# Performance work log

Measured on AMD Instinct MI355X. Metric: run time of the kernel, lower is better.

The kernel has to match this reference:

```python
import jax, jax.numpy as jnp
import numpy as np

B, T, I, H, O = 128, 512, 256, 512, 256


def setup_inputs() -> dict:
    key = jax.random.key(0)
    ks = jax.random.split(key, 12)
    s = 1.0 / np.sqrt(H)  # torch nn.GRUCell/Linear-style uniform init scale
    u = lambda k, shape: jax.random.uniform(k, shape, jnp.float32, -s, s)
    return {
        "x": jax.random.normal(ks[0], (B, T, I), jnp.float32),
        "h0": jax.random.normal(ks[1], (B, H), jnp.float32),
        "W_ih0": u(ks[2], (3 * H, I)),
        "W_hh0": u(ks[3], (3 * H, H)),
        "b_ih0": u(ks[4], (3 * H,)),
        "b_hh0": u(ks[5], (3 * H,)),
        "W_ih1": u(ks[6], (3 * H, H)),
        "W_hh1": u(ks[7], (3 * H, H)),
        "b_ih1": u(ks[8], (3 * H,)),
        "b_hh1": u(ks[9], (3 * H,)),
        "W_out": u(ks[10], (O, H)),
        "b_out": u(ks[11], (O,)),
    }


def _cell(inp, h, W_ih, W_hh, b_ih, b_hh):
    # Standard GRU cell (PyTorch gate order: r, z, n)
    gi = inp @ W_ih.T + b_ih  # [B, 3H]
    gh = h @ W_hh.T + b_hh    # [B, 3H]
    i_r, i_z, i_n = jnp.split(gi, 3, axis=-1)
    h_r, h_z, h_n = jnp.split(gh, 3, axis=-1)
    r = jax.nn.sigmoid(i_r + h_r)
    z = jax.nn.sigmoid(i_z + h_z)
    n = jnp.tanh(i_n + r * h_n)
    return (1.0 - z) * n + z * h


def reference(x, h0, W_ih0, W_hh0, b_ih0, b_hh0, W_ih1, W_hh1, b_ih1, b_hh1, W_out, b_out):
    def step(h, x_t):
        h = _cell(x_t, h, W_ih0, W_hh0, b_ih0, b_hh0)
        # Source quirk: a SINGLE hidden state is shared across stacked layers,
        # so layer 1 receives h both as input and as previous hidden state.
        h = _cell(h, h, W_ih1, W_hh1, b_ih1, b_hh1)
        y = h @ W_out.T + b_out  # [B, O]
        return h, y

    _, Y = jax.lax.scan(step, h0, jnp.swapaxes(x, 0, 1))  # Y: [T, B, O]
    return jnp.swapaxes(Y, 0, 1)  # [B, T, O]
```

## Files before the change

### kernel.cpp

```cpp
#include <hip/hip_runtime.h>


typedef short s16x8 __attribute__((ext_vector_type(8)));
typedef float f32x4 __attribute__((ext_vector_type(4)));
typedef unsigned short u16;
typedef unsigned int u32;

#define MFMA(a, b, c) __builtin_amdgcn_mfma_f32_16x16x32_bf16((a), (b), (c), 0, 0, 0)

static constexpr int NBLK = 128;
static constexpr int LDS_WROWS = 112;
static constexpr int LDS_STRIDE = 520;
static constexpr int LDS_BYTES = LDS_WROWS * LDS_STRIDE * 2 + 2 * 512 * 4;
static constexpr int OFF_FA = 0, OFF_FB = 8192, OFF_GA = 16384, OFF_GB = 17408;
static constexpr int FLAGS_U32 = 18432;

__device__ __forceinline__ u16 f2bf(float f) {
  unsigned u = __builtin_bit_cast(unsigned, f);
  u = u + 0x7fffu + ((u >> 16) & 1u);
  return (u16)(u >> 16);
}
__device__ __forceinline__ float sigm(float x) { return 1.f / (1.f + __expf(-x)); }
__device__ __forceinline__ float tanh_f(float x) { return 1.f - 2.f / (1.f + __expf(2.f * x)); }

__device__ __forceinline__ s16x8 scload16(const u16* p) {
  s16x8 v;
  asm volatile("global_load_dwordx4 %0, %1, off sc0 sc1" : "=v"(v) : "v"(p));
  return v;
}
__device__ __forceinline__ void scstore_u16(u16* p, u16 v) {
  unsigned vv = v;
  asm volatile("global_store_short %0, %1, off sc0 sc1" :: "v"(p), "v"(vv) : "memory");
}
__device__ __forceinline__ u32 scload_u32(const u32* p) {
  u32 v;
  asm volatile("global_load_dword %0, %1, off sc0 sc1\n\ts_waitcnt vmcnt(0)"
               : "=v"(v) : "v"(p) : "memory");
  return v;
}
__device__ __forceinline__ void scstore_u32(u32* p, u32 v) {
  asm volatile("global_store_dword %0, %1, off sc0 sc1" :: "v"(p), "v"(v) : "memory");
}
#define VWAIT0()                                        \
  do {                                                  \
    asm volatile("s_waitcnt vmcnt(0)" ::: "memory");    \
    __builtin_amdgcn_sched_barrier(0);                  \
  } while (0)
#define DRAIN_ALL()                                              \
  do {                                                           \
    asm volatile("s_waitcnt vmcnt(0) lgkmcnt(0)" ::: "memory");  \
    __builtin_amdgcn_sched_barrier(0);                           \
  } while (0)

__device__ __forceinline__ void gather64(const u32* base, u32 val, int l) {
  for (;;) {
    u32 v = scload_u32(base + l * 32);
    if (__all(v >= val)) break;
    __builtin_amdgcn_s_sleep(2);
  }
}
__device__ __forceinline__ void pollgo(const u32* p, u32 val) {
  for (;;) {
    u32 v = scload_u32(p);
    if (v >= val) break;
    __builtin_amdgcn_s_sleep(4);
  }
}

__global__ void prep_kernel(const float* __restrict__ W_ih0, const float* __restrict__ W_hh0,
                            const float* __restrict__ W_ih1, const float* __restrict__ W_hh1,
                            const float* __restrict__ W_out, const float* __restrict__ h0,
                            u16* __restrict__ WL0, u16* __restrict__ WL1,
                            u16* __restrict__ WOB, u16* __restrict__ ring1,
                            u32* __restrict__ flags) {
  const int n0 = 1536 * 768, n1 = 2048 * 512, n2 = 256 * 512, n3 = 128 * 512;
  const int total = n0 + n1 + n2 + n3 + FLAGS_U32;
  for (int i = blockIdx.x * blockDim.x + threadIdx.x; i < total; i += gridDim.x * blockDim.x) {
    if (i < n0) {
      int row = i / 768, c = i % 768;
      float v = (c < 256) ? W_ih0[row * 256 + c] : W_hh0[row * 512 + (c - 256)];
      WL0[i] = f2bf(v);
    } else if (i < n0 + n1) {
      int k2 = i - n0;
      int row = k2 / 512, k = k2 % 512;
      int strip = row >> 9, j = row & 511;
      float v;
      if (strip == 0)      v = W_ih1[j * 512 + k] + W_hh1[j * 512 + k];
      else if (strip == 1) v = W_ih1[(512 + j) * 512 + k] + W_hh1[(512 + j) * 512 + k];
      else if (strip == 2) v = W_ih1[(1024 + j) * 512 + k];
      else                 v = W_hh1[(1024 + j) * 512 + k];
      WL1[k2] = f2bf(v);
    } else if (i < n0 + n1 + n2) {
      int k2 = i - n0 - n1;
      WOB[k2] = f2bf(W_out[k2]);
    } else if (i < n0 + n1 + n2 + n3) {
      int k2 = i - n0 - n1 - n2;
      ring1[k2] = f2bf(h0[k2]);
    } else {
      flags[i - n0 - n1 - n2 - n3] = 0u;
    }
  }
}

__global__ __launch_bounds__(256) void gru_persist(
    const float* __restrict__ x, const float* __restrict__ h0,
    const float* __restrict__ b_ih0, const float* __restrict__ b_hh0,
    const float* __restrict__ b_ih1, const float* __restrict__ b_hh1,
    const float* __restrict__ b_out,
    const u16* __restrict__ WL0, const u16* __restrict__ WL1, const u16* __restrict__ WOB,
    u16* __restrict__ ring,
    u16* __restrict__ hlb,
    float* __restrict__ Y, u32* __restrict__ flags) {
  extern __shared__ u16 smem[];
  float* h_f32  = (float*)(smem + LDS_WROWS * LDS_STRIDE);
  float* hl_f32 = h_f32 + 512;

  const int blk = blockIdx.x;
  const int m = blk >> 5;
  const int s = blk & 31;
  const int w = threadIdx.x >> 6, l = threadIdx.x & 63;
  const int l15 = l & 15, l4 = l >> 4;

  for (int idx = threadIdx.x; idx < LDS_WROWS * 512; idx += 256) {
    int row = idx >> 9, k = idx & 511;
    u16 v;
    if (row < 48) {
      int g = row >> 4, jj = row & 15;
      v = WL0[(size_t)(g * 512 + s * 16 + jj) * 768 + 256 + k];
    } else {
      int rr = row - 48, g = rr >> 4, jj = rr & 15;
      v = WL1[(size_t)(g * 512 + s * 16 + jj) * 512 + k];
    }
    smem[row * LDS_STRIDE + k] = v;
  }
  for (int idx = threadIdx.x; idx < 512; idx += 256) {
    int rr = idx >> 4, cc = idx & 15;
    h_f32[idx] = h0[(size_t)(32 * m + rr) * 512 + s * 16 + cc];
  }
  __syncthreads();

  const int jg = s * 16 + l15;
  const float br0 = b_ih0[jg] + b_hh0[jg];
  const float bz0 = b_ih0[512 + jg] + b_hh0[512 + jg];
  const float bni0 = b_ih0[1024 + jg], bnh0 = b_hh0[1024 + jg];
  const float br1 = b_ih1[jg] + b_hh1[jg];
  const float bz1 = b_ih1[512 + jg] + b_hh1[512 + jg];
  const float bni1 = b_ih1[1024 + jg], bnh1 = b_hh1[1024 + jg];

  const u16* wxr = WL0 + (size_t)jg * 768 + l4 * 8;
  const u16* wxz = WL0 + (size_t)(512 + jg) * 768 + l4 * 8;
  const u16* wxn = WL0 + (size_t)(1024 + jg) * 768 + l4 * 8;
  const u16* lr  = smem + (0 * 16 + l15) * LDS_STRIDE + l4 * 8;
  const u16* lz  = smem + (1 * 16 + l15) * LDS_STRIDE + l4 * 8;
  const u16* ln  = smem + (2 * 16 + l15) * LDS_STRIDE + l4 * 8;
  const u16* m10 = smem + (48 + 0 * 16 + l15) * LDS_STRIDE + l4 * 8;
  const u16* m11 = smem + (48 + 1 * 16 + l15) * LDS_STRIDE + l4 * 8;
  const u16* m12 = smem + (48 + 2 * 16 + l15) * LDS_STRIDE + l4 * 8;
  const u16* m13 = smem + (48 + 3 * 16 + l15) * LDS_STRIDE + l4 * 8;

  u32* fA = flags + OFF_FA + m * 2048;
  u32* fB = flags + OFF_FB + m * 2048;
  u32* gA = flags + OFF_GA + m * 256;
  u32* gB = flags + OFF_GB + m * 256;

  if (w < 2) {
    const int amt = w;
    const int arow = 32 * m + amt * 16 + l15;
    u32* myfA = fA + (s * 2 + amt) * 32;
    const u32* mygo = gB + (s & 7) * 32;
    const int yo = (s & 15) * 16 + l15;
    const float ybo = b_out[yo];
    const u16* ywv = WOB + (size_t)yo * 512 + l4 * 8;

    for (int t = 0; t < 512; ++t) {
      const u16* ringc = ring + (size_t)((t + 1) & 1) * 65536;

      if (t > 0) {
        if (s == 0) {
          gather64(fB, (u32)t, l);
          if (w == 0 && l < 8) scstore_u32(gB + l * 32, (u32)t);
        } else {
          pollgo(mygo, (u32)t);
        }
        __builtin_amdgcn_sched_barrier(0);
      }

      s16x8 hb[16];
      const u16* hr = ringc + (size_t)arow * 512 + l4 * 8;
      #pragma unroll
      for (int kt = 0; kt < 16; ++kt) hb[kt] = scload16(hr + kt * 32);

      f32x4 aR = {0,0,0,0}, aZ = {0,0,0,0}, aNI = {0,0,0,0}, aNH = {0,0,0,0};
      const float* xr = x + ((size_t)arow * 512 + t) * 256 + l4 * 8;
      #pragma unroll
      for (int kt = 0; kt < 8; ++kt) {
        float4 u = *(const float4*)(xr + kt * 32);
        float4 v = *(const float4*)(xr + kt * 32 + 4);
        s16x8 a;
        a[0]=f2bf(u.x); a[1]=f2bf(u.y); a[2]=f2bf(u.z); a[3]=f2bf(u.w);
        a[4]=f2bf(v.x); a[5]=f2bf(v.y); a[6]=f2bf(v.z); a[7]=f2bf(v.w);
        aR  = MFMA(a, *(const s16x8*)(wxr + kt * 32), aR);
        aZ  = MFMA(a, *(const s16x8*)(wxz + kt * 32), aZ);
        aNI = MFMA(a, *(const s16x8*)(wxn + kt * 32), aNI);
      }
      VWAIT0();
      #pragma unroll
      for (int kt = 0; kt < 16; ++kt) {
        aR  = MFMA(hb[kt], *(const s16x8*)(lr + kt * 32), aR);
        aZ  = MFMA(hb[kt], *(const s16x8*)(lz + kt * 32), aZ);
        aNH = MFMA(hb[kt], *(const s16x8*)(ln + kt * 32), aNH);
      }

      #pragma unroll
      for (int j = 0; j < 4; ++j) {
        int rr = amt * 16 + l4 * 4 + j;
        float r = sigm(aR[j] + br0), z = sigm(aZ[j] + bz0);
        float n = tanh_f(aNI[j] + bni0 + r * (aNH[j] + bnh0));
        float h = (1.f - z) * n + z * h_f32[rr * 16 + l15];
        hl_f32[rr * 16 + l15] = h;
        scstore_u16(hlb + (size_t)(32 * m + rr) * 512 + jg, f2bf(h));
      }
      DRAIN_ALL();
      if (l == 0) scstore_u32(myfA, (u32)(t + 1));

      if (s < 16 && t > 0) {
        f32x4 acc = {0,0,0,0};
        #pragma unroll
        for (int kt = 0; kt < 16; ++kt)
          acc = MFMA(hb[kt], *(const s16x8*)(ywv + kt * 32), acc);
        #pragma unroll
        for (int j = 0; j < 4; ++j)
          Y[((size_t)(32 * m + amt * 16 + l4 * 4 + j) * 512 + (t - 1)) * 256 + yo]
              = acc[j] + ybo;
      }
    }

    if (s == 0) {
      gather64(fB, 512u, l);
      if (w == 0 && l < 8) scstore_u32(gB + l * 32, 512u);
    } else {
      pollgo(mygo, 512u);
    }
    if (s < 16) {
      const u16* Hf = ring + 65536;
      s16x8 yb[16];
      const u16* ar = Hf + (size_t)arow * 512 + l4 * 8;
      #pragma unroll
      for (int kt = 0; kt < 16; ++kt) yb[kt] = scload16(ar + kt * 32);
      VWAIT0();
      f32x4 acc = {0,0,0,0};
      #pragma unroll
      for (int kt = 0; kt < 16; ++kt)
        acc = MFMA(yb[kt], *(const s16x8*)(ywv + kt * 32), acc);
      #pragma unroll
      for (int j = 0; j < 4; ++j)
        Y[((size_t)(32 * m + amt * 16 + l4 * 4 + j) * 512 + 511) * 256 + yo]
            = acc[j] + ybo;
    }
  } else {
    const int bmt = w - 2;
    const int brow = 32 * m + bmt * 16 + l15;
    u32* myfB = fB + (s * 2 + bmt) * 32;
    const u32* mygo = gA + (s & 7) * 32;

    for (int t = 0; t < 512; ++t) {
      u16* ringn = ring + (size_t)(t & 1) * 65536;

      if (s == 0) {
        gather64(fA, (u32)(t + 1), l);
        if (w == 2 && l < 8) scstore_u32(gA + l * 32, (u32)(t + 1));
      } else {
        pollgo(mygo, (u32)(t + 1));
      }
      __builtin_amdgcn_sched_barrier(0);

      s16x8 pb[16];
      const u16* ar = hlb + (size_t)brow * 512 + l4 * 8;
      #pragma unroll
      for (int kt = 0; kt < 16; ++kt) pb[kt] = scload16(ar + kt * 32);
      VWAIT0();
      f32x4 cR = {0,0,0,0}, cZ = {0,0,0,0}, cNI = {0,0,0,0}, cNH = {0,0,0,0};
      #pragma unroll
      for (int kt = 0; kt < 16; ++kt) {
        cR  = MFMA(pb[kt], *(const s16x8*)(m10 + kt * 32), cR);
        cZ  = MFMA(pb[kt], *(const s16x8*)(m11 + kt * 32), cZ);
        cNI = MFMA(pb[kt], *(const s16x8*)(m12 + kt * 32), cNI);
        cNH = MFMA(pb[kt], *(const s16x8*)(m13 + kt * 32), cNH);
      }
      #pragma unroll
      for (int j = 0; j < 4; ++j) {
        int rr = bmt * 16 + l4 * 4 + j;
        float r = sigm(cR[j] + br1), z = sigm(cZ[j] + bz1);
        float n = tanh_f(cNI[j] + bni1 + r * (cNH[j] + bnh1));
        float h = (1.f - z) * n + z * hl_f32[rr * 16 + l15];
        h_f32[rr * 16 + l15] = h;
        scstore_u16(ringn + (size_t)(32 * m + rr) * 512 + jg, f2bf(h));
      }
      DRAIN_ALL();
      if (l == 0) scstore_u32(myfB, (u32)(t + 1));
    }
  }
}

extern "C" void kernel_launch(void* const* d_in, const int* in_sizes, int n_in,
                              void* d_out, int out_size, void* d_ws, size_t ws_size,
                              hipStream_t stream) {
  const float* x     = (const float*)d_in[0];
  const float* h0    = (const float*)d_in[1];
  const float* W_ih0 = (const float*)d_in[2];
  const float* W_hh0 = (const float*)d_in[3];
  const float* b_ih0 = (const float*)d_in[4];
  const float* b_hh0 = (const float*)d_in[5];
  const float* W_ih1 = (const float*)d_in[6];
  const float* W_hh1 = (const float*)d_in[7];
  const float* b_ih1 = (const float*)d_in[8];
  const float* b_hh1 = (const float*)d_in[9];
  const float* W_out = (const float*)d_in[10];
  const float* b_out = (const float*)d_in[11];
  float* Y = (float*)d_out;

  u32* flags = (u32*)d_ws;
  u16* WL0  = (u16*)(flags + FLAGS_U32);
  u16* WL1  = WL0 + 1536 * 768;
  u16* WOB  = WL1 + 2048 * 512;
  u16* ring = WOB + 256 * 512;
  u16* hlb  = ring + 2 * 65536;

  (void)hipFuncSetAttribute((const void*)gru_persist,
                            hipFuncAttributeMaxDynamicSharedMemorySize, LDS_BYTES);

  prep_kernel<<<dim3(1024), dim3(256), 0, stream>>>(W_ih0, W_hh0, W_ih1, W_hh1,
                                                    W_out, h0, WL0, WL1, WOB,
                                                    ring + 65536, flags);
  gru_persist<<<dim3(NBLK), dim3(256), LDS_BYTES, stream>>>(
      x, h0, b_ih0, b_hh0, b_ih1, b_hh1, b_out, WL0, WL1, WOB,
      ring, hlb, Y, flags);
}
```

Baseline: 5.639 ms.

## Split cross-block sync flags per 16-row tile and overlap output GEMM

Sync flags become per 16-row tile instead of per 32-row group. Each tile now waits only on the 32 producers that wrote its own rows, rather than on all 64 producers across both tiles. The output projection MFMA is moved ahead of the drain and flag store so it can overlap with the in-flight h stores, and the go-flag poll sleep is shortened. This relaxes the coupling between the two tiles in a group, at the cost of more flag memory and more polling traffic.

```diff
diff --git a/kernel.cpp b/kernel.cpp
--- a/kernel.cpp
+++ b/kernel.cpp
@@ -12,8 +12,11 @@
 static constexpr int LDS_WROWS = 112;
 static constexpr int LDS_STRIDE = 520;
 static constexpr int LDS_BYTES = LDS_WROWS * LDS_STRIDE * 2 + 2 * 512 * 4;
-static constexpr int OFF_FA = 0, OFF_FB = 8192, OFF_GA = 16384, OFF_GB = 17408;
-static constexpr int FLAGS_U32 = 18432;
+static constexpr int OFF_FA = 0;
+static constexpr int OFF_FB = 8192;
+static constexpr int OFF_GA = 16384;
+static constexpr int OFF_GB = 18432;
+static constexpr int FLAGS_U32 = 20480;
 
 __device__ __forceinline__ u16 f2bf(float f) {
   unsigned u = __builtin_bit_cast(unsigned, f);
@@ -52,10 +55,14 @@
     __builtin_amdgcn_sched_barrier(0);                           \
   } while (0)
 
-__device__ __forceinline__ void gather64(const u32* base, u32 val, int l) {
+__device__ __forceinline__ void gather32(const u32* base, u32 val, int l) {
   for (;;) {
-    u32 v = scload_u32(base + l * 32);
-    if (__all(v >= val)) break;
+    int ok = 1;
+    if (l < 32) {
+      u32 v = scload_u32(base + l * 32);
+      ok = (v >= val) ? 1 : 0;
+    }
+    if (__all(ok)) break;
     __builtin_amdgcn_s_sleep(2);
   }
 }
@@ -63,7 +70,7 @@
   for (;;) {
     u32 v = scload_u32(p);
     if (v >= val) break;
-    __builtin_amdgcn_s_sleep(4);
+    __builtin_amdgcn_s_sleep(2);
   }
 }
 
@@ -158,16 +165,14 @@
   const u16* m12 = smem + (48 + 2 * 16 + l15) * LDS_STRIDE + l4 * 8;
   const u16* m13 = smem + (48 + 3 * 16 + l15) * LDS_STRIDE + l4 * 8;
 
-  u32* fA = flags + OFF_FA + m * 2048;
-  u32* fB = flags + OFF_FB + m * 2048;
-  u32* gA = flags + OFF_GA + m * 256;
-  u32* gB = flags + OFF_GB + m * 256;
-
   if (w < 2) {
-    const int amt = w;
-    const int arow = 32 * m + amt * 16 + l15;
-    u32* myfA = fA + (s * 2 + amt) * 32;
-    const u32* mygo = gB + (s & 7) * 32;
+    const int tl = w;
+    const int arow = 32 * m + tl * 16 + l15;
+    u32* fAt = flags + OFF_FA + (m * 2 + tl) * 1024;
+    u32* fBt = flags + OFF_FB + (m * 2 + tl) * 1024;
+    u32* gBt = flags + OFF_GB + (m * 2 + tl) * 256;
+    u32* myfA = fAt + s * 32;
+    const u32* mygo = gBt + (s & 7) * 32;
     const int yo = (s & 15) * 16 + l15;
     const float ybo = b_out[yo];
     const u16* ywv = WOB + (size_t)yo * 512 + l4 * 8;
@@ -177,8 +182,8 @@
 
       if (t > 0) {
         if (s == 0) {
-          gather64(fB, (u32)t, l);
-          if (w == 0 && l < 8) scstore_u32(gB + l * 32, (u32)t);
+          gather32(fBt, (u32)t, l);
+          if (l < 8) scstore_u32(gBt + l * 32, (u32)t);
         } else {
           pollgo(mygo, (u32)t);
         }
@@ -213,31 +218,34 @@
 
       #pragma unroll
       for (int j = 0; j < 4; ++j) {
-        int rr = amt * 16 + l4 * 4 + j;
+        int rr = tl * 16 + l4 * 4 + j;
         float r = sigm(aR[j] + br0), z = sigm(aZ[j] + bz0);
         float n = tanh_f(aNI[j] + bni0 + r * (aNH[j] + bnh0));
         float h = (1.f - z) * n + z * h_f32[rr * 16 + l15];
         hl_f32[rr * 16 + l15] = h;
         scstore_u16(hlb + (size_t)(32 * m + rr) * 512 + jg, f2bf(h));
       }
+
+      f32x4 yacc = {0,0,0,0};
+      if (s < 16 && t > 0) {
+        #pragma unroll
+        for (int kt = 0; kt < 16; ++kt)
+          yacc = MFMA(hb[kt], *(const s16x8*)(ywv + kt * 32), yacc);
+      }
       DRAIN_ALL();
       if (l == 0) scstore_u32(myfA, (u32)(t + 1));
 
       if (s < 16 && t > 0) {
-        f32x4 acc = {0,0,0,0};
-        #pragma unroll
-        for (int kt = 0; kt < 16; ++kt)
-          acc = MFMA(hb[kt], *(const s16x8*)(ywv + kt * 32), acc);
         #pragma unroll
         for (int j = 0; j < 4; ++j)
-          Y[((size_t)(32 * m + amt * 16 + l4 * 4 + j) * 512 + (t - 1)) * 256 + yo]
-              = acc[j] + ybo;
+          Y[((size_t)(32 * m + tl * 16 + l4 * 4 + j) * 512 + (t - 1)) * 256 + yo]
+              = yacc[j] + ybo;
       }
     }
 
     if (s == 0) {
-      gather64(fB, 512u, l);
-      if (w == 0 && l < 8) scstore_u32(gB + l * 32, 512u);
+      gather32(fBt, 512u, l);
+      if (l < 8) scstore_u32(gBt + l * 32, 512u);
     } else {
       pollgo(mygo, 512u);
     }
@@ -254,21 +262,24 @@
         acc = MFMA(yb[kt], *(const s16x8*)(ywv + kt * 32), acc);
       #pragma unroll
       for (int j = 0; j < 4; ++j)
-        Y[((size_t)(32 * m + amt * 16 + l4 * 4 + j) * 512 + 511) * 256 + yo]
+        Y[((size_t)(32 * m + tl * 16 + l4 * 4 + j) * 512 + 511) * 256 + yo]
             = acc[j] + ybo;
     }
   } else {
-    const int bmt = w - 2;
-    const int brow = 32 * m + bmt * 16 + l15;
-    u32* myfB = fB + (s * 2 + bmt) * 32;
-    const u32* mygo = gA + (s & 7) * 32;
+    const int tl = w - 2;
+    const int brow = 32 * m + tl * 16 + l15;
+    u32* fAt = flags + OFF_FA + (m * 2 + tl) * 1024;
+    u32* fBt = flags + OFF_FB + (m * 2 + tl) * 1024;
+    u32* gAt = flags + OFF_GA + (m * 2 + tl) * 256;
+    u32* myfB = fBt + s * 32;
+    const u32* mygo = gAt + (s & 7) * 32;
 
     for (int t = 0; t < 512; ++t) {
       u16* ringn = ring + (size_t)(t & 1) * 65536;
 
       if (s == 0) {
-        gather64(fA, (u32)(t + 1), l);
-        if (w == 2 && l < 8) scstore_u32(gA + l * 32, (u32)(t + 1));
+        gather32(fAt, (u32)(t + 1), l);
+        if (l < 8) scstore_u32(gAt + l * 32, (u32)(t + 1));
       } else {
         pollgo(mygo, (u32)(t + 1));
       }
@@ -289,7 +300,7 @@
       }
       #pragma unroll
       for (int j = 0; j < 4; ++j) {
-        int rr = bmt * 16 + l4 * 4 + j;
+        int rr = tl * 16 + l4 * 4 + j;
         float r = sigm(cR[j] + br1), z = sigm(cZ[j] + bz1);
         float n = tanh_f(cNI[j] + bni1 + r * (cNH[j] + bnh1));
         float h = (1.f - z) * n + z * hl_f32[rr * 16 + l15];
```

Result: slower. 6.018 ms (+6.7%).

## Precompute next-step input projection off the critical path and pack hidden-state stores

Applied to the files above, without the earlier changes.

The layer-0 input projection (x_t · W_ih0) for step t+1 is now computed after the step-t flag has been published, so it no longer sits between the go-signal and the recurrent MFMAs. Hidden-state writes go through a per-tile LDS buffer and are repacked into 8-byte bf16 stores, replacing many 2-byte system-coherent stores. The output-projection MFMAs are issued before the drain wait, so they overlap the store latency. The polling sleep interval is also shortened. The cost is extra LDS traffic and registers held across the loop, plus some leftover dead variables.

```diff
diff --git a/kernel.cpp b/kernel.cpp
--- a/kernel.cpp
+++ b/kernel.cpp
@@ -3,6 +3,7 @@
 
 typedef short s16x8 __attribute__((ext_vector_type(8)));
 typedef float f32x4 __attribute__((ext_vector_type(4)));
+typedef unsigned int u32x2 __attribute__((ext_vector_type(2)));
 typedef unsigned short u16;
 typedef unsigned int u32;
 
@@ -28,9 +29,8 @@
   asm volatile("global_load_dwordx4 %0, %1, off sc0 sc1" : "=v"(v) : "v"(p));
   return v;
 }
-__device__ __forceinline__ void scstore_u16(u16* p, u16 v) {
-  unsigned vv = v;
-  asm volatile("global_store_short %0, %1, off sc0 sc1" :: "v"(p), "v"(vv) : "memory");
+__device__ __forceinline__ void scstore8(u16* p, u32x2 v) {
+  asm volatile("global_store_dwordx2 %0, %1, off sc0 sc1" :: "v"(p), "v"(v) : "memory");
 }
 __device__ __forceinline__ u32 scload_u32(const u32* p) {
   u32 v;
@@ -53,8 +53,9 @@
   } while (0)
 
 __device__ __forceinline__ void gather64(const u32* base, u32 val, int l) {
+  const u32* p = base + l * 32;
   for (;;) {
-    u32 v = scload_u32(base + l * 32);
+    u32 v = scload_u32(p);
     if (__all(v >= val)) break;
     __builtin_amdgcn_s_sleep(2);
   }
@@ -63,7 +64,7 @@
   for (;;) {
     u32 v = scload_u32(p);
     if (v >= val) break;
-    __builtin_amdgcn_s_sleep(4);
+    __builtin_amdgcn_s_sleep(2);
   }
 }
 
@@ -135,7 +136,8 @@
   }
   for (int idx = threadIdx.x; idx < 512; idx += 256) {
     int rr = idx >> 4, cc = idx & 15;
-    h_f32[idx] = h0[(size_t)(32 * m + rr) * 512 + s * 16 + cc];
+    int tl0 = rr >> 4, rl = rr & 15;
+    h_f32[tl0 * 256 + rl * 16 + cc] = h0[(size_t)(32 * m + rr) * 512 + s * 16 + cc];
   }
   __syncthreads();
 
@@ -158,19 +160,38 @@
   const u16* m12 = smem + (48 + 2 * 16 + l15) * LDS_STRIDE + l4 * 8;
   const u16* m13 = smem + (48 + 3 * 16 + l15) * LDS_STRIDE + l4 * 8;
 
+  const int tr = l >> 2, tc = (l & 3) * 4;
+
   u32* fA = flags + OFF_FA + m * 2048;
   u32* fB = flags + OFF_FB + m * 2048;
   u32* gA = flags + OFF_GA + m * 256;
   u32* gB = flags + OFF_GB + m * 256;
 
   if (w < 2) {
-    const int amt = w;
-    const int arow = 32 * m + amt * 16 + l15;
-    u32* myfA = fA + (s * 2 + amt) * 32;
+    const int tl = w;
+    const int arow = 32 * m + tl * 16 + l15;
+    u32* myfA = fA + (s * 2 + tl) * 32;
     const u32* mygo = gB + (s & 7) * 32;
     const int yo = (s & 15) * 16 + l15;
     const float ybo = b_out[yo];
     const u16* ywv = WOB + (size_t)yo * 512 + l4 * 8;
+    float* hlT = hl_f32 + tl * 256;
+    float* hT  = h_f32 + tl * 256;
+    u16* hlb_dst = hlb + (size_t)(32 * m + tl * 16 + tr) * 512 + s * 16 + tc;
+    const float* xrow = x + (size_t)arow * 512 * 256 + l4 * 8;
+
+    f32x4 aR = {0,0,0,0}, aZ = {0,0,0,0}, aNI = {0,0,0,0};
+    #pragma unroll
+    for (int kt = 0; kt < 8; ++kt) {
+      float4 u = *(const float4*)(xrow + kt * 32);
+      float4 v = *(const float4*)(xrow + kt * 32 + 4);
+      s16x8 a;
+      a[0]=f2bf(u.x); a[1]=f2bf(u.y); a[2]=f2bf(u.z); a[3]=f2bf(u.w);
+      a[4]=f2bf(v.x); a[5]=f2bf(v.y); a[6]=f2bf(v.z); a[7]=f2bf(v.w);
+      aR  = MFMA(a, *(const s16x8*)(wxr + kt * 32), aR);
+      aZ  = MFMA(a, *(const s16x8*)(wxz + kt * 32), aZ);
+      aNI = MFMA(a, *(const s16x8*)(wxn + kt * 32), aNI);
+    }
 
     for (int t = 0; t < 512; ++t) {
       const u16* ringc = ring + (size_t)((t + 1) & 1) * 65536;
@@ -189,21 +210,8 @@
       const u16* hr = ringc + (size_t)arow * 512 + l4 * 8;
       #pragma unroll
       for (int kt = 0; kt < 16; ++kt) hb[kt] = scload16(hr + kt * 32);
-
-      f32x4 aR = {0,0,0,0}, aZ = {0,0,0,0}, aNI = {0,0,0,0}, aNH = {0,0,0,0};
-      const float* xr = x + ((size_t)arow * 512 + t) * 256 + l4 * 8;
-      #pragma unroll
-      for (int kt = 0; kt < 8; ++kt) {
-        float4 u = *(const float4*)(xr + kt * 32);
-        float4 v = *(const float4*)(xr + kt * 32 + 4);
-        s16x8 a;
-        a[0]=f2bf(u.x); a[1]=f2bf(u.y); a[2]=f2bf(u.z); a[3]=f2bf(u.w);
-        a[4]=f2bf(v.x); a[5]=f2bf(v.y); a[6]=f2bf(v.z); a[7]=f2bf(v.w);
-        aR  = MFMA(a, *(const s16x8*)(wxr + kt * 32), aR);
-        aZ  = MFMA(a, *(const s16x8*)(wxz + kt * 32), aZ);
-        aNI = MFMA(a, *(const s16x8*)(wxn + kt * 32), aNI);
-      }
       VWAIT0();
+      f32x4 aNH = {0,0,0,0};
       #pragma unroll
       for (int kt = 0; kt < 16; ++kt) {
         aR  = MFMA(hb[kt], *(const s16x8*)(lr + kt * 32), aR);
@@ -213,25 +221,48 @@
 
       #pragma unroll
       for (int j = 0; j < 4; ++j) {
-        int rr = amt * 16 + l4 * 4 + j;
+        int rl = l4 * 4 + j;
         float r = sigm(aR[j] + br0), z = sigm(aZ[j] + bz0);
         float n = tanh_f(aNI[j] + bni0 + r * (aNH[j] + bnh0));
-        float h = (1.f - z) * n + z * h_f32[rr * 16 + l15];
-        hl_f32[rr * 16 + l15] = h;
-        scstore_u16(hlb + (size_t)(32 * m + rr) * 512 + jg, f2bf(h));
+        hlT[rl * 16 + l15] = (1.f - z) * n + z * hT[rl * 16 + l15];
+      }
+      {
+        float4 hv = *(const float4*)&hlT[tr * 16 + tc];
+        u32x2 pk;
+        pk.x = ((u32)f2bf(hv.y) << 16) | f2bf(hv.x);
+        pk.y = ((u32)f2bf(hv.w) << 16) | f2bf(hv.z);
+        scstore8(hlb_dst, pk);
+      }
+
+      f32x4 yacc = {0,0,0,0};
+      if (s < 16 && t > 0) {
+        #pragma unroll
+        for (int kt = 0; kt < 16; ++kt)
+          yacc = MFMA(hb[kt], *(const s16x8*)(ywv + kt * 32), yacc);
       }
       DRAIN_ALL();
       if (l == 0) scstore_u32(myfA, (u32)(t + 1));
 
       if (s < 16 && t > 0) {
-        f32x4 acc = {0,0,0,0};
-        #pragma unroll
-        for (int kt = 0; kt < 16; ++kt)
-          acc = MFMA(hb[kt], *(const s16x8*)(ywv + kt * 32), acc);
         #pragma unroll
         for (int j = 0; j < 4; ++j)
-          Y[((size_t)(32 * m + amt * 16 + l4 * 4 + j) * 512 + (t - 1)) * 256 + yo]
-              = acc[j] + ybo;
+          Y[((size_t)(32 * m + tl * 16 + l4 * 4 + j) * 512 + (t - 1)) * 256 + yo]
+              = yacc[j] + ybo;
+      }
+      if (t < 511) {
+        const float* xr = xrow + (size_t)(t + 1) * 256;
+        aR = (f32x4){0,0,0,0}; aZ = (f32x4){0,0,0,0}; aNI = (f32x4){0,0,0,0};
+        #pragma unroll
+        for (int kt = 0; kt < 8; ++kt) {
+          float4 u = *(const float4*)(xr + kt * 32);
+          float4 v = *(const float4*)(xr + kt * 32 + 4);
+          s16x8 a;
+          a[0]=f2bf(u.x); a[1]=f2bf(u.y); a[2]=f2bf(u.z); a[3]=f2bf(u.w);
+          a[4]=f2bf(v.x); a[5]=f2bf(v.y); a[6]=f2bf(v.z); a[7]=f2bf(v.w);
+          aR  = MFMA(a, *(const s16x8*)(wxr + kt * 32), aR);
+          aZ  = MFMA(a, *(const s16x8*)(wxz + kt * 32), aZ);
+          aNI = MFMA(a, *(const s16x8*)(wxn + kt * 32), aNI);
+        }
       }
     }
 
@@ -254,17 +285,22 @@
         acc = MFMA(yb[kt], *(const s16x8*)(ywv + kt * 32), acc);
       #pragma unroll
       for (int j = 0; j < 4; ++j)
-        Y[((size_t)(32 * m + amt * 16 + l4 * 4 + j) * 512 + 511) * 256 + yo]
+        Y[((size_t)(32 * m + tl * 16 + l4 * 4 + j) * 512 + 511) * 256 + yo]
             = acc[j] + ybo;
     }
   } else {
-    const int bmt = w - 2;
-    const int brow = 32 * m + bmt * 16 + l15;
-    u32* myfB = fB + (s * 2 + bmt) * 32;
+    const int tl = w - 2;
+    const int brow = 32 * m + tl * 16 + l15;
+    u32* myfB = fB + (s * 2 + tl) * 32;
     const u32* mygo = gA + (s & 7) * 32;
+    float* hlT = hl_f32 + tl * 256;
+    float* hT  = h_f32 + tl * 256;
+    u16* ring_dst_base = (u16*)0;
+    const size_t dst_off = (size_t)(32 * m + tl * 16 + tr) * 512 + s * 16 + tc;
 
     for (int t = 0; t < 512; ++t) {
       u16* ringn = ring + (size_t)(t & 1) * 65536;
+      (void)ring_dst_base;
 
       if (s == 0) {
         gather64(fA, (u32)(t + 1), l);
@@ -289,12 +325,19 @@
       }
       #pragma unroll
       for (int j = 0; j < 4; ++j) {
-        int rr = bmt * 16 + l4 * 4 + j;
+        int rl = tl ? 0 : 0;
+        (void)rl;
+        int rloc = l4 * 4 + j;
         float r = sigm(cR[j] + br1), z = sigm(cZ[j] + bz1);
         float n = tanh_f(cNI[j] + bni1 + r * (cNH[j] + bnh1));
-        float h = (1.f - z) * n + z * hl_f32[rr * 16 + l15];
-        h_f32[rr * 16 + l15] = h;
-        scstore_u16(ringn + (size_t)(32 * m + rr) * 512 + jg, f2bf(h));
+        hT[rloc * 16 + l15] = (1.f - z) * n + z * hlT[rloc * 16 + l15];
+      }
+      {
+        float4 hv = *(const float4*)&hT[tr * 16 + tc];
+        u32x2 pk;
+        pk.x = ((u32)f2bf(hv.y) << 16) | f2bf(hv.x);
+        pk.y = ((u32)f2bf(hv.w) << 16) | f2bf(hv.z);
+        scstore8(ringn + dst_off, pk);
       }
       DRAIN_ALL();
       if (l == 0) scstore_u32(myfB, (u32)(t + 1));
```

New measurement: 6.364 ms. 12.9% more time.
